# Kernel tuning notes

Hardware: AMD Instinct MI355X
Metric: run time of the kernel (lower is better)

The kernel has to match this reference:

```python
import jax, jax.numpy as jnp
import numpy as np

MEM_SIZE = 2048
CELL = 64
R_HEADS = 4
IN_SIZE = 512
IFACE = CELL * R_HEADS + CELL + 2 * CELL + 2 * R_HEADS + 5  # 461
DELTA = 1e-6
EPS = 1e-6


def setup_inputs() -> dict:
    key = jax.random.key(0)
    ks = jax.random.split(key, 8)
    b = 256
    return {
        'xi': jax.random.normal(ks[0], (b, IN_SIZE), jnp.float32),
        'W': jax.random.normal(ks[1], (IFACE, IN_SIZE), jnp.float32) * 0.05,
        'gamma': jnp.ones((IFACE,), jnp.float32),
        'beta': jnp.zeros((IFACE,), jnp.float32),
        'memory': jax.random.normal(ks[2], (b, MEM_SIZE, CELL), jnp.float32),
        'read_weights': jax.random.uniform(ks[3], (b, R_HEADS, MEM_SIZE), jnp.float32),
        'write_weights': jax.random.uniform(ks[4], (b, 1, MEM_SIZE), jnp.float32),
        'usage': jax.random.uniform(ks[5], (b, MEM_SIZE), jnp.float32),
    }


def _cosine(mem, keys):
    # mem: (b,m,c), keys: (b,k,c) -> (b,k,m)
    mem_n = mem / (jnp.linalg.norm(mem, axis=-1, keepdims=True) + EPS)
    key_n = keys / (jnp.linalg.norm(keys, axis=-1, keepdims=True) + EPS)
    return jnp.einsum('bkc,bmc->bkm', key_n, mem_n)


def reference(xi, W, gamma, beta, memory, read_weights, write_weights, usage):
    b = xi.shape[0]
    r, k, w, m = R_HEADS, CELL, CELL, MEM_SIZE

    # interface projection + GroupNorm(1, C) over channel dim
    itf = xi @ W.T
    mu = jnp.mean(itf, axis=1, keepdims=True)
    var = jnp.var(itf, axis=1, keepdims=True)
    itf = (itf - mu) / jnp.sqrt(var + 1e-5) * gamma + beta

    c = 0
    read_keys = jnp.tanh(itf[:, c:c + r * k].reshape(b, r, k)); c += r * k
    read_strengths = jax.nn.softplus(itf[:, c:c + r]); c += r
    write_key = jnp.tanh(itf[:, c:c + k].reshape(b, 1, k)); c += k
    write_strength = jax.nn.softplus(itf[:, c]).reshape(b, 1); c += 1
    erase_vec = jax.nn.sigmoid(itf[:, c:c + w].reshape(b, 1, w)); c += w
    write_vec = jnp.tanh(itf[:, c:c + w].reshape(b, 1, w)); c += w
    free_gates = jax.nn.sigmoid(itf[:, c:c + r]); c += r
    alloc_gate = jax.nn.softmax(itf[:, c:c + 3], axis=1); c += 3
    write_gate = jax.nn.sigmoid(itf[:, c]).reshape(b, 1)

    # ---- usage update ----
    u = usage + (1 - usage) * (1 - jnp.prod(1 - write_weights, axis=1))
    psi = jnp.prod(1 - free_gates[:, :, None] * read_weights, axis=1)  # (b,m)
    u = u * psi

    # ---- content weighting for write ----
    wcw = jax.nn.softmax(_cosine(memory, write_key) * write_strength[:, :, None], axis=2)  # (b,1,m)

    # ---- allocation ----
    u2 = DELTA + (1 - DELTA) * u
    idx = jnp.argsort(u2, axis=1)                              # ascending usage (phi)
    su = jnp.take_along_axis(u2, idx, axis=1)                  # sorted usage
    cp = jnp.cumprod(jnp.concatenate([jnp.ones((b, 1), u2.dtype), su], axis=1), axis=1)[:, :-1]
    sa = (1 - su) * cp
    inv = jnp.argsort(idx, axis=1)                             # inverse permutation (phi_rev)
    alloc = jnp.take_along_axis(sa, inv, axis=1)               # (b,m)

    # ---- write weighting ----
    fw = (alloc_gate[:, 0:1] * jnp.mean(read_weights, axis=1)
          + alloc_gate[:, 1:2] * alloc
          + alloc_gate[:, 2:3] * wcw[:, 0])
    ww = (write_gate * fw)[:, None, :]                         # (b,1,m)

    # ---- memory write (erase + add) ----
    reset_gate = jnp.prod(1 - ww[:, :, :, None] * erase_vec[:, :, None, :], axis=1)  # (b,m,w)
    mem = memory * reset_gate + jnp.einsum('bm,bw->bmw', ww[:, 0], write_vec[:, 0])

    # ---- read ----
    rw = jax.nn.softmax(_cosine(mem, read_keys) * read_strengths[:, :, None], axis=2)  # (b,r,m)
    read_vectors = jnp.einsum('brm,bmw->brw', rw, mem)         # (b,r,w)
    return read_vectors
```

## Files before the change

### kernel.cpp

```cpp
#include <hip/hip_runtime.h>
#include <math.h>

#define MM    2048
#define CC    64
#define RH    4
#define NIF   461
#define INS   512
#define EPSN  1e-6f

typedef unsigned long long u64;

#define OFF_P     ((size_t)0)
#define OFF_U2    ((size_t)131072)
#define OFF_MRW   ((size_t)655360)
#define OFF_SC    ((size_t)1179648)
#define OFF_ALLOC ((size_t)1703936)
#define OFF_WW    ((size_t)2228224)
#define OFF_PART  ((size_t)2752512)
#define OFF_PSTAT ((size_t)3276800)

__global__ __launch_bounds__(512) void k1_interface(
    const float* __restrict__ xi, const float* __restrict__ W,
    const float* __restrict__ gamma, const float* __restrict__ beta,
    const float* __restrict__ read_w, const float* __restrict__ write_w,
    const float* __restrict__ usage, float* __restrict__ ws)
{
  const int b = blockIdx.x, tid = threadIdx.x;
  const int lane = tid & 63, wid = tid >> 6;
  __shared__ __align__(16) float s_xi[512], s_itf[512], s_act[512];
  __shared__ float sRed[24];

  s_xi[tid] = xi[(size_t)b*INS + tid];
  __syncthreads();

  {
    const float4 x0 = ((const float4*)s_xi)[lane*2];
    const float4 x1 = ((const float4*)s_xi)[lane*2+1];
    for (int col = wid; col < NIF; col += 8) {
      const float4* Wr = (const float4*)(W + (size_t)col*INS);
      float4 a0 = Wr[lane*2], a1 = Wr[lane*2+1];
      float p = a0.x*x0.x + a0.y*x0.y + a0.z*x0.z + a0.w*x0.w
              + a1.x*x1.x + a1.y*x1.y + a1.z*x1.z + a1.w*x1.w;
      #pragma unroll
      for (int off=1; off<64; off<<=1) p += __shfl_xor(p, off);
      if (lane==0) s_itf[col] = p;
    }
  }
  __syncthreads();

  {
    float v = (tid < NIF) ? s_itf[tid] : 0.f;
    float s = v, q = v*v;
    #pragma unroll
    for (int off=1; off<64; off<<=1) { s += __shfl_xor(s,off); q += __shfl_xor(q,off); }
    if (lane==0){ sRed[wid] = s; sRed[8+wid] = q; }
    __syncthreads();
    if (tid==0){
      float ts=0.f, tq=0.f;
      for (int i=0;i<8;i++){ ts+=sRed[i]; tq+=sRed[8+i]; }
      float mean = ts/(float)NIF;
      float var  = tq/(float)NIF - mean*mean;
      sRed[16]=mean; sRed[17]=rsqrtf(var+1e-5f);
    }
    __syncthreads();
    float mean = sRed[16], rstd = sRed[17];
    if (tid < NIF) {
      float g = (s_itf[tid]-mean)*rstd*gamma[tid] + beta[tid];
      float a;
      if      (tid < 256) a = tanhf(g);
      else if (tid < 260) a = fmaxf(g,0.f) + log1pf(expf(-fabsf(g)));
      else if (tid < 324) a = tanhf(g);
      else if (tid ==324) a = fmaxf(g,0.f) + log1pf(expf(-fabsf(g)));
      else if (tid < 389) a = 1.f/(1.f+expf(-g));
      else if (tid < 453) a = tanhf(g);
      else if (tid < 457) a = 1.f/(1.f+expf(-g));
      else if (tid < 460) a = g;
      else                a = 1.f/(1.f+expf(-g));
      s_act[tid] = a;
    }
  }
  __syncthreads();

  float* P = ws + OFF_P + (size_t)b*512;
  if (wid < 4) {
    float t = s_act[wid*64 + lane];
    float q = t*t;
    #pragma unroll
    for (int off=1; off<64; off<<=1) q += __shfl_xor(q,off);
    P[wid*64+lane] = t * (s_act[256+wid] / (sqrtf(q) + EPSN));
  } else if (wid == 4) {
    float t = s_act[260+lane];
    float q = t*t;
    #pragma unroll
    for (int off=1; off<64; off<<=1) q += __shfl_xor(q,off);
    P[256+lane] = t * (s_act[324] / (sqrtf(q) + EPSN));
  } else if (wid == 5) {
    P[320+lane] = s_act[325+lane];
    P[384+lane] = s_act[389+lane];
  } else if (wid == 6 && lane == 0) {
    float a0=s_act[457], a1=s_act[458], a2=s_act[459];
    float mx = fmaxf(a0, fmaxf(a1,a2));
    float e0=expf(a0-mx), e1=expf(a1-mx), e2=expf(a2-mx);
    float is = 1.f/(e0+e1+e2);
    P[448]=e0*is; P[449]=e1*is; P[450]=e2*is; P[451]=s_act[460];
  }

  {
    const float4* us4 = (const float4*)(usage   + (size_t)b*MM);
    const float4* wr4 = (const float4*)(write_w + (size_t)b*MM);
    const float4* rw4 = (const float4*)(read_w  + (size_t)b*RH*MM);
    const float fg0=s_act[453], fg1=s_act[454], fg2=s_act[455], fg3=s_act[456];
    float4 u = us4[tid], w = wr4[tid];
    float4 r0 = rw4[tid], r1 = rw4[512+tid], r2 = rw4[1024+tid], r3 = rw4[1536+tid];
    float4 mr, u2o;
    mr.x = 0.25f*(r0.x+r1.x+r2.x+r3.x);
    mr.y = 0.25f*(r0.y+r1.y+r2.y+r3.y);
    mr.z = 0.25f*(r0.z+r1.z+r2.z+r3.z);
    mr.w = 0.25f*(r0.w+r1.w+r2.w+r3.w);
    #define U2C(comp)                                                           \
    { float uu  = u.comp + (1.f-u.comp)*w.comp;                                 \
      float psi = (1.f-fg0*r0.comp)*(1.f-fg1*r1.comp)*(1.f-fg2*r2.comp)*(1.f-fg3*r3.comp); \
      u2o.comp = 1e-6f + (1.f-1e-6f)*(uu*psi); }
    U2C(x) U2C(y) U2C(z) U2C(w)
    #undef U2C
    ((float4*)(ws + OFF_MRW + (size_t)b*MM))[tid] = mr;
    ((float4*)(ws + OFF_U2  + (size_t)b*MM))[tid] = u2o;
  }
}

__global__ __launch_bounds__(256) void k2_fused(
    const float* __restrict__ memory, float* __restrict__ ws)
{
  __shared__ __align__(16) u64 sKeys[2048];
  __shared__ float sT[260];
  const int tid = threadIdx.x;

  if (blockIdx.x < 256) {
    const int b = blockIdx.x;
    const int lane = tid & 63, w = tid >> 6;
    const float* u2p = ws + OFF_U2 + (size_t)b*MM;
    for (int i = tid; i < MM; i += 256)
      sKeys[i] = ((u64)__float_as_uint(u2p[i])<<32) | (unsigned)i;
    __syncthreads();

    for (int k = 2; k <= MM; k <<= 1) {
      for (int j = k >> 1; j > 0; j >>= 1) {
        #pragma unroll 4
        for (int c = tid; c < MM/2; c += 256) {
          int i   = ((c & ~(j-1)) << 1) | (c & (j-1));
          int ixj = i | j;
          u64 a = sKeys[i], d = sKeys[ixj];
          bool up = ((i & k) == 0);
          if ((a > d) == up) { sKeys[i] = d; sKeys[ixj] = a; }
        }
        __syncthreads();
      }
    }

    float p[8];
    {
      float run = 1.f;
      #pragma unroll
      for (int e = 0; e < 8; ++e) {
        float su = __uint_as_float((unsigned)(sKeys[tid*8+e]>>32));
        run *= su; p[e] = run;
      }
      sT[tid] = run;
    }
    __syncthreads();
    float v = sT[tid];
    float incl = v;
    #pragma unroll
    for (int off=1; off<64; off<<=1) {
      float n = __shfl_up(incl, off);
      if (lane >= off) incl *= n;
    }
    float excl = __shfl_up(incl, 1);
    if (lane == 0) excl = 1.f;
    if (lane == 63) sT[256 + w] = incl;
    __syncthreads();
    float base = 1.f;
    for (int ww2 = 0; ww2 < w; ++ww2) base *= sT[256 + ww2];
    float E = base * excl;

    float* allocp = ws + OFF_ALLOC + (size_t)b*MM;
    #pragma unroll
    for (int e = 0; e < 8; ++e) {
      u64 kk = sKeys[tid*8+e];
      float su = __uint_as_float((unsigned)(kk>>32));
      unsigned idx = (unsigned)(kk & 0xFFFFFFFFu);
      float cp = E * (e ? p[e-1] : 1.f);
      allocp[idx] = (1.f - su) * cp;
    }
  } else {
    const int f = blockIdx.x - 256;
    const int b = f >> 3, slice = f & 7;
    const int l16 = tid & 15, rowg = tid >> 4;
    const float* P = ws + OFF_P + (size_t)b*512;
    const float4 wk4 = ((const float4*)(P+256))[l16];
    const float4* mem4 = (const float4*)(memory + (size_t)b*MM*CC) + (size_t)slice*256*16;
    float* sc = ws + OFF_SC + (size_t)b*MM + slice*256;
    #pragma unroll 4
    for (int it = 0; it < 16; ++it) {
      int m = it*16 + rowg;
      float4 vv = mem4[m*16 + l16];
      float d = vv.x*wk4.x + vv.y*wk4.y + vv.z*wk4.z + vv.w*wk4.w;
      float q = vv.x*vv.x + vv.y*vv.y + vv.z*vv.z + vv.w*vv.w;
      #pragma unroll
      for (int off=1; off<16; off<<=1){ d += __shfl_xor(d,off); q += __shfl_xor(q,off); }
      if (l16==0) sc[m] = d / (sqrtf(q)+EPSN);
    }
  }
}

__global__ __launch_bounds__(256) void k3_ww(float* __restrict__ ws)
{
  const int b = blockIdx.x, tid = threadIdx.x;
  const int lane = tid & 63, w = tid >> 6;
  __shared__ float sR[8];
  const float4* sc4 = (const float4*)(ws + OFF_SC + (size_t)b*MM);
  float4 v0 = sc4[tid*2], v1 = sc4[tid*2+1];
  float m = fmaxf(fmaxf(fmaxf(v0.x,v0.y),fmaxf(v0.z,v0.w)),
                  fmaxf(fmaxf(v1.x,v1.y),fmaxf(v1.z,v1.w)));
  #pragma unroll
  for (int off=1; off<64; off<<=1) m = fmaxf(m, __shfl_xor(m,off));
  if (lane==0) sR[w] = m;
  __syncthreads();
  m = fmaxf(fmaxf(sR[0],sR[1]), fmaxf(sR[2],sR[3]));
  float e0=expf(v0.x-m), e1=expf(v0.y-m), e2=expf(v0.z-m), e3=expf(v0.w-m);
  float e4=expf(v1.x-m), e5=expf(v1.y-m), e6=expf(v1.z-m), e7=expf(v1.w-m);
  float s = e0+e1+e2+e3+e4+e5+e6+e7;
  #pragma unroll
  for (int off=1; off<64; off<<=1) s += __shfl_xor(s,off);
  if (lane==0) sR[4+w] = s;
  __syncthreads();
  float inv = 1.f/(sR[4]+sR[5]+sR[6]+sR[7]);

  const float* P = ws + OFF_P + (size_t)b*512;
  const float ag0=P[448], ag1=P[449], ag2=P[450], wg=P[451];
  const float4* mr4 = (const float4*)(ws + OFF_MRW   + (size_t)b*MM);
  const float4* al4 = (const float4*)(ws + OFF_ALLOC + (size_t)b*MM);
  float4* ww4 = (float4*)(ws + OFF_WW + (size_t)b*MM);
  float4 mra = mr4[tid*2], mrb = mr4[tid*2+1];
  float4 ala = al4[tid*2], alb = al4[tid*2+1];
  float4 oa, ob;
  oa.x = wg*(ag0*mra.x + ag1*ala.x + ag2*e0*inv);
  oa.y = wg*(ag0*mra.y + ag1*ala.y + ag2*e1*inv);
  oa.z = wg*(ag0*mra.z + ag1*ala.z + ag2*e2*inv);
  oa.w = wg*(ag0*mra.w + ag1*ala.w + ag2*e3*inv);
  ob.x = wg*(ag0*mrb.x + ag1*alb.x + ag2*e4*inv);
  ob.y = wg*(ag0*mrb.y + ag1*alb.y + ag2*e5*inv);
  ob.z = wg*(ag0*mrb.z + ag1*alb.z + ag2*e6*inv);
  ob.w = wg*(ag0*mrb.w + ag1*alb.w + ag2*e7*inv);
  ww4[tid*2] = oa; ww4[tid*2+1] = ob;
}

__global__ __launch_bounds__(256) void k4_passB(
    const float* __restrict__ memory, float* __restrict__ ws)
{
  const int slice = blockIdx.x, b = blockIdx.y;
  const int tid = threadIdx.x, l16 = tid & 15, rowg = tid >> 4;
  const int lane = tid & 63, wid = tid >> 6;
  __shared__ __align__(16) float chunk[64*68];
  __shared__ __align__(16) float sE[4*68];
  __shared__ float sHm[4], sHs[4], sHsc[4];

  const float* P = ws + OFF_P + (size_t)b*512;
  const float4 er4 = ((const float4*)(P+320))[l16];
  const float4 wv4 = ((const float4*)(P+384))[l16];
  const float4 k0 = ((const float4*)P)[     l16];
  const float4 k1 = ((const float4*)P)[16 + l16];
  const float4 k2 = ((const float4*)P)[32 + l16];
  const float4 k3 = ((const float4*)P)[48 + l16];
  const float* wwp = ws + OFF_WW + (size_t)b*MM + slice*256;
  const float4* mem4 = (const float4*)(memory + (size_t)b*MM*CC) + (size_t)slice*256*16;

  if (tid < 4){ sHm[tid] = -INFINITY; sHs[tid] = 0.f; }
  __syncthreads();
  const int q = lane & 15, ps = lane >> 4;
  float4 acc; acc.x=acc.y=acc.z=acc.w=0.f;

  for (int ch = 0; ch < 4; ++ch) {
    #pragma unroll
    for (int pp = 0; pp < 4; ++pp) {
      int p = pp*16 + rowg;
      int m = ch*64 + p;
      float4 v = mem4[m*16 + l16];
      float wm = wwp[m];
      float4 nv;
      nv.x = v.x*(1.f - wm*er4.x) + wm*wv4.x;
      nv.y = v.y*(1.f - wm*er4.y) + wm*wv4.y;
      nv.z = v.z*(1.f - wm*er4.z) + wm*wv4.z;
      nv.w = v.w*(1.f - wm*er4.w) + wm*wv4.w;
      *(float4*)&chunk[p*68 + (l16<<2)] = nv;
      float d0 = nv.x*k0.x+nv.y*k0.y+nv.z*k0.z+nv.w*k0.w;
      float d1 = nv.x*k1.x+nv.y*k1.y+nv.z*k1.z+nv.w*k1.w;
      float d2 = nv.x*k2.x+nv.y*k2.y+nv.z*k2.z+nv.w*k2.w;
      float d3 = nv.x*k3.x+nv.y*k3.y+nv.z*k3.z+nv.w*k3.w;
      float qq = nv.x*nv.x+nv.y*nv.y+nv.z*nv.z+nv.w*nv.w;
      #pragma unroll
      for (int off=1; off<16; off<<=1){
        d0+=__shfl_xor(d0,off); d1+=__shfl_xor(d1,off);
        d2+=__shfl_xor(d2,off); d3+=__shfl_xor(d3,off);
        qq+=__shfl_xor(qq,off);
      }
      if (l16==0){
        float inv = 1.f/(sqrtf(qq)+EPSN);
        sE[      p] = d0*inv;
        sE[ 68 + p] = d1*inv;
        sE[136 + p] = d2*inv;
        sE[204 + p] = d3*inv;
      }
    }
    __syncthreads();
    {
      float v = sE[wid*68 + lane];
      float cm = v;
      #pragma unroll
      for (int off=1; off<64; off<<=1) cm = fmaxf(cm, __shfl_xor(cm,off));
      float om = sHm[wid];
      float nm = fmaxf(om, cm);
      float scl = expf(om - nm);
      float e = expf(v - nm);
      sE[wid*68 + lane] = e;
      float es = e;
      #pragma unroll
      for (int off=1; off<64; off<<=1) es += __shfl_xor(es,off);
      if (lane==0){
        sHs[wid] = sHs[wid]*scl + es;
        sHm[wid] = nm;
        sHsc[wid] = scl;
      }
    }
    __syncthreads();
    {
      float scl = sHsc[wid];
      acc.x*=scl; acc.y*=scl; acc.z*=scl; acc.w*=scl;
      #pragma unroll
      for (int pp = 0; pp < 16; ++pp) {
        int p = ps*16 + pp;
        float e = sE[wid*68 + p];
        const float4 mv = *(const float4*)&chunk[p*68 + (q<<2)];
        acc.x += e*mv.x; acc.y += e*mv.y; acc.z += e*mv.z; acc.w += e*mv.w;
      }
    }
    __syncthreads();
  }

  #pragma unroll
  for (int off=16; off<64; off<<=1) {
    acc.x += __shfl_xor(acc.x, off);
    acc.y += __shfl_xor(acc.y, off);
    acc.z += __shfl_xor(acc.z, off);
    acc.w += __shfl_xor(acc.w, off);
  }
  if (ps == 0) {
    float* pacc = ws + OFF_PART + ((((size_t)b*8 + slice)*4 + wid)<<6);
    *(float4*)&pacc[q<<2] = acc;
  }
  if (lane == 0) {
    float* pst = ws + OFF_PSTAT + (((size_t)b*8 + slice)*4 + wid)*2;
    pst[0] = sHm[wid]; pst[1] = sHs[wid];
  }
}

__global__ __launch_bounds__(256) void k5_combine(
    const float* __restrict__ ws, float* __restrict__ out)
{
  const int b = blockIdx.x, tid = threadIdx.x;
  const int head = tid >> 6, c = tid & 63;
  float M = -INFINITY;
  #pragma unroll
  for (int s = 0; s < 8; ++s)
    M = fmaxf(M, ws[OFF_PSTAT + (((size_t)b*8 + s)*4 + head)*2]);
  float S = 0.f, A = 0.f;
  #pragma unroll
  for (int s = 0; s < 8; ++s) {
    const float* pst = ws + OFF_PSTAT + (((size_t)b*8 + s)*4 + head)*2;
    float w = expf(pst[0] - M);
    S += w * pst[1];
    A += w * ws[OFF_PART + ((((size_t)b*8 + s)*4 + head)<<6) + c];
  }
  out[((size_t)b<<8) + head*64 + c] = A / S;
}

extern "C" void kernel_launch(void* const* d_in, const int* in_sizes, int n_in,
                              void* d_out, int out_size, void* d_ws, size_t ws_size,
                              hipStream_t stream) {
  const float* xi      = (const float*)d_in[0];
  const float* W       = (const float*)d_in[1];
  const float* gamma   = (const float*)d_in[2];
  const float* beta    = (const float*)d_in[3];
  const float* memory  = (const float*)d_in[4];
  const float* read_w  = (const float*)d_in[5];
  const float* write_w = (const float*)d_in[6];
  const float* usage   = (const float*)d_in[7];
  float* ws  = (float*)d_ws;
  float* out = (float*)d_out;

  k1_interface<<<dim3(256), dim3(512), 0, stream>>>(xi, W, gamma, beta, read_w, write_w, usage, ws);
  k2_fused   <<<dim3(2304), dim3(256), 0, stream>>>(memory, ws);
  k3_ww      <<<dim3(256), dim3(256), 0, stream>>>(ws);
  k4_passB   <<<dim3(8,256), dim3(256), 0, stream>>>(memory, ws);
  k5_combine <<<dim3(256), dim3(256), 0, stream>>>(ws, out);
}
```

Baseline: 132.3 us.

## Precompute per-row dot products to derive post-write cosine scores algebraically

The memory-scan kernel now computes, for each memory row, a set of dot products (row with write key, erase-weighted row, write vector and read keys). These let the written memory's norms and read-key cosines be reconstructed from the write weight without building the new memory. A single per-batch kernel then does the full read softmax exactly instead of an online softmax across slices. The final pass becomes a plain weighted reduction of the original memory, and the erase/add terms are applied algebraically in the combine step. This moves arithmetic out of the second memory pass at the cost of a larger per-row scalar buffer and more dot products in the first pass.

```diff
diff --git a/kernel.cpp b/kernel.cpp
--- a/kernel.cpp
+++ b/kernel.cpp
@@ -13,11 +13,11 @@
 #define OFF_P     ((size_t)0)
 #define OFF_U2    ((size_t)131072)
 #define OFF_MRW   ((size_t)655360)
-#define OFF_SC    ((size_t)1179648)
-#define OFF_ALLOC ((size_t)1703936)
-#define OFF_WW    ((size_t)2228224)
-#define OFF_PART  ((size_t)2752512)
-#define OFF_PSTAT ((size_t)3276800)
+#define OFF_ALLOC ((size_t)1179648)
+#define OFF_SCAL  ((size_t)1703936)
+#define OFF_W8    ((size_t)10092544)
+#define OFF_CR    ((size_t)14286848)
+#define OFF_PART  ((size_t)14287872)
 
 __global__ __launch_bounds__(512) void k1_interface(
     const float* __restrict__ xi, const float* __restrict__ W,
@@ -195,172 +195,252 @@
   } else {
     const int f = blockIdx.x - 256;
     const int b = f >> 3, slice = f & 7;
-    const int l16 = tid & 15, rowg = tid >> 4;
+    const int q = tid & 7, rowg = tid >> 3;
     const float* P = ws + OFF_P + (size_t)b*512;
-    const float4 wk4 = ((const float4*)(P+256))[l16];
+    const float4 wkA = ((const float4*)(P+256))[q*2], wkB = ((const float4*)(P+256))[q*2+1];
+    const float4 eA  = ((const float4*)(P+320))[q*2], eB  = ((const float4*)(P+320))[q*2+1];
+    const float4 wvA = ((const float4*)(P+384))[q*2], wvB = ((const float4*)(P+384))[q*2+1];
+    const float4 k0A = ((const float4*)P)[      q*2], k0B = ((const float4*)P)[      q*2+1];
+    const float4 k1A = ((const float4*)P)[ 16 + q*2], k1B = ((const float4*)P)[ 16 + q*2+1];
+    const float4 k2A = ((const float4*)P)[ 32 + q*2], k2B = ((const float4*)P)[ 32 + q*2+1];
+    const float4 k3A = ((const float4*)P)[ 48 + q*2], k3B = ((const float4*)P)[ 48 + q*2+1];
     const float4* mem4 = (const float4*)(memory + (size_t)b*MM*CC) + (size_t)slice*256*16;
-    float* sc = ws + OFF_SC + (size_t)b*MM + slice*256;
-    #pragma unroll 4
-    for (int it = 0; it < 16; ++it) {
-      int m = it*16 + rowg;
-      float4 vv = mem4[m*16 + l16];
-      float d = vv.x*wk4.x + vv.y*wk4.y + vv.z*wk4.z + vv.w*wk4.w;
-      float q = vv.x*vv.x + vv.y*vv.y + vv.z*vv.z + vv.w*vv.w;
+    float4* sc4 = (float4*)(ws + OFF_SCAL) + ((size_t)b*MM + slice*256)*4;
+
+    for (int it = 0; it < 8; ++it) {
+      int m = it*32 + rowg;
+      float4 vA = mem4[m*16 + q*2], vB = mem4[m*16 + q*2+1];
+      float4 veA, veB;
+      veA.x=vA.x*eA.x; veA.y=vA.y*eA.y; veA.z=vA.z*eA.z; veA.w=vA.w*eA.w;
+      veB.x=vB.x*eB.x; veB.y=vB.y*eB.y; veB.z=vB.z*eB.z; veB.w=vB.w*eB.w;
+      #define DOT(a,b) (a.x*b.x + a.y*b.y + a.z*b.z + a.w*b.w)
+      float S  = DOT(vA,wkA) + DOT(vB,wkB);
+      float A  = DOT(vA,vA)  + DOT(vB,vB);
+      float B  = DOT(veA,vA) + DOT(veB,vB);
+      float C  = DOT(veA,veA)+ DOT(veB,veB);
+      float D  = DOT(vA,wvA) + DOT(vB,wvB);
+      float E  = DOT(veA,wvA)+ DOT(veB,wvB);
+      float G0 = DOT(vA,k0A) + DOT(vB,k0B);
+      float G1 = DOT(vA,k1A) + DOT(vB,k1B);
+      float G2 = DOT(vA,k2A) + DOT(vB,k2B);
+      float G3 = DOT(vA,k3A) + DOT(vB,k3B);
+      float H0 = DOT(veA,k0A)+ DOT(veB,k0B);
+      float H1 = DOT(veA,k1A)+ DOT(veB,k1B);
+      float H2 = DOT(veA,k2A)+ DOT(veB,k2B);
+      float H3 = DOT(veA,k3A)+ DOT(veB,k3B);
+      #undef DOT
       #pragma unroll
-      for (int off=1; off<16; off<<=1){ d += __shfl_xor(d,off); q += __shfl_xor(q,off); }
-      if (l16==0) sc[m] = d / (sqrtf(q)+EPSN);
-    }
-  }
-}
-
-__global__ __launch_bounds__(256) void k3_ww(float* __restrict__ ws)
+      for (int off=1; off<8; off<<=1) {
+        S += __shfl_xor(S,off);   A += __shfl_xor(A,off);
+        B += __shfl_xor(B,off);   C += __shfl_xor(C,off);
+        D += __shfl_xor(D,off);   E += __shfl_xor(E,off);
+        G0 += __shfl_xor(G0,off); G1 += __shfl_xor(G1,off);
+        G2 += __shfl_xor(G2,off); G3 += __shfl_xor(G3,off);
+        H0 += __shfl_xor(H0,off); H1 += __shfl_xor(H1,off);
+        H2 += __shfl_xor(H2,off); H3 += __shfl_xor(H3,off);
+      }
+      if (q == 0) {
+        float4 o0; o0.x=S;  o0.y=A;  o0.z=B;  o0.w=C;
+        float4 o1; o1.x=D;  o1.y=E;  o1.z=0;  o1.w=0;
+        float4 o2; o2.x=G0; o2.y=G1; o2.z=G2; o2.w=G3;
+        float4 o3; o3.x=H0; o3.y=H1; o3.z=H2; o3.w=H3;
+        sc4[m*4+0]=o0; sc4[m*4+1]=o1; sc4[m*4+2]=o2; sc4[m*4+3]=o3;
+      }
+    }
+  }
+}
+
+__global__ __launch_bounds__(256) void k3_weights(float* __restrict__ ws)
 {
   const int b = blockIdx.x, tid = threadIdx.x;
   const int lane = tid & 63, w = tid >> 6;
-  __shared__ float sR[8];
-  const float4* sc4 = (const float4*)(ws + OFF_SC + (size_t)b*MM);
-  float4 v0 = sc4[tid*2], v1 = sc4[tid*2+1];
-  float m = fmaxf(fmaxf(fmaxf(v0.x,v0.y),fmaxf(v0.z,v0.w)),
-                  fmaxf(fmaxf(v1.x,v1.y),fmaxf(v1.z,v1.w)));
-  #pragma unroll
-  for (int off=1; off<64; off<<=1) m = fmaxf(m, __shfl_xor(m,off));
-  if (lane==0) sR[w] = m;
-  __syncthreads();
-  m = fmaxf(fmaxf(sR[0],sR[1]), fmaxf(sR[2],sR[3]));
-  float e0=expf(v0.x-m), e1=expf(v0.y-m), e2=expf(v0.z-m), e3=expf(v0.w-m);
-  float e4=expf(v1.x-m), e5=expf(v1.y-m), e6=expf(v1.z-m), e7=expf(v1.w-m);
-  float s = e0+e1+e2+e3+e4+e5+e6+e7;
-  #pragma unroll
-  for (int off=1; off<64; off<<=1) s += __shfl_xor(s,off);
-  if (lane==0) sR[4+w] = s;
-  __syncthreads();
-  float inv = 1.f/(sR[4]+sR[5]+sR[6]+sR[7]);
+  __shared__ float sWraw[2048];
+  __shared__ float sWw[2048];
+  __shared__ float sSc[4*2048];
+  __shared__ float sR[64];
+  __shared__ float sKF[8];
 
   const float* P = ws + OFF_P + (size_t)b*512;
+  const float* scal = ws + OFF_SCAL + (size_t)b*MM*16;
+  const float4* sc4 = (const float4*)scal;
+
+  if (tid < 64) {
+    float wv = P[384+tid];
+    float p0=wv*P[tid], p1=wv*P[64+tid], p2=wv*P[128+tid], p3=wv*P[192+tid], f=wv*wv;
+    #pragma unroll
+    for (int off=1; off<64; off<<=1) {
+      p0+=__shfl_xor(p0,off); p1+=__shfl_xor(p1,off); p2+=__shfl_xor(p2,off);
+      p3+=__shfl_xor(p3,off); f+=__shfl_xor(f,off);
+    }
+    if (tid==0){ sKF[0]=p0; sKF[1]=p1; sKF[2]=p2; sKF[3]=p3; sKF[4]=f; }
+  }
+  __syncthreads();
+
+  float lm = -INFINITY;
+  #pragma unroll
+  for (int k = 0; k < 8; ++k) {
+    int m = tid + k*256;
+    float4 s0 = sc4[m*4];
+    float wraw = s0.x / (sqrtf(s0.y)+EPSN);
+    sWraw[m] = wraw;
+    lm = fmaxf(lm, wraw);
+  }
+  #pragma unroll
+  for (int off=1; off<64; off<<=1) lm = fmaxf(lm, __shfl_xor(lm,off));
+  if (lane==0) sR[w] = lm;
+  __syncthreads();
+  const float Mw = fmaxf(fmaxf(sR[0],sR[1]), fmaxf(sR[2],sR[3]));
+  float ls = 0.f;
+  #pragma unroll
+  for (int k = 0; k < 8; ++k) ls += expf(sWraw[tid + k*256] - Mw);
+  #pragma unroll
+  for (int off=1; off<64; off<<=1) ls += __shfl_xor(ls,off);
+  if (lane==0) sR[4+w] = ls;
+  __syncthreads();
+  const float invW = 1.f/(sR[4]+sR[5]+sR[6]+sR[7]);
+
   const float ag0=P[448], ag1=P[449], ag2=P[450], wg=P[451];
-  const float4* mr4 = (const float4*)(ws + OFF_MRW   + (size_t)b*MM);
-  const float4* al4 = (const float4*)(ws + OFF_ALLOC + (size_t)b*MM);
-  float4* ww4 = (float4*)(ws + OFF_WW + (size_t)b*MM);
-  float4 mra = mr4[tid*2], mrb = mr4[tid*2+1];
-  float4 ala = al4[tid*2], alb = al4[tid*2+1];
-  float4 oa, ob;
-  oa.x = wg*(ag0*mra.x + ag1*ala.x + ag2*e0*inv);
-  oa.y = wg*(ag0*mra.y + ag1*ala.y + ag2*e1*inv);
-  oa.z = wg*(ag0*mra.z + ag1*ala.z + ag2*e2*inv);
-  oa.w = wg*(ag0*mra.w + ag1*ala.w + ag2*e3*inv);
-  ob.x = wg*(ag0*mrb.x + ag1*alb.x + ag2*e4*inv);
-  ob.y = wg*(ag0*mrb.y + ag1*alb.y + ag2*e5*inv);
-  ob.z = wg*(ag0*mrb.z + ag1*alb.z + ag2*e6*inv);
-  ob.w = wg*(ag0*mrb.w + ag1*alb.w + ag2*e7*inv);
-  ww4[tid*2] = oa; ww4[tid*2+1] = ob;
-}
-
-__global__ __launch_bounds__(256) void k4_passB(
-    const float* __restrict__ memory, float* __restrict__ ws)
+  const float K0=sKF[0], K1=sKF[1], K2=sKF[2], K3=sKF[3], F=sKF[4];
+  const float* mrwp = ws + OFF_MRW   + (size_t)b*MM;
+  const float* alp  = ws + OFF_ALLOC + (size_t)b*MM;
+
+  float hm0=-INFINITY, hm1=-INFINITY, hm2=-INFINITY, hm3=-INFINITY;
+  #pragma unroll
+  for (int k = 0; k < 8; ++k) {
+    int m = tid + k*256;
+    float wcw = expf(sWraw[m]-Mw)*invW;
+    float wwv = wg*(ag0*mrwp[m] + ag1*alp[m] + ag2*wcw);
+    sWw[m] = wwv;
+    float4 s0 = sc4[m*4], s1 = sc4[m*4+1], sG = sc4[m*4+2], sH = sc4[m*4+3];
+    float nsq = s0.y + 2.f*wwv*(s1.x - s0.z) + wwv*wwv*(s0.w - 2.f*s1.y + F);
+    float rstd = 1.f/(sqrtf(fmaxf(nsq,0.f))+EPSN);
+    float c0 = (sG.x + wwv*(K0 - sH.x))*rstd;
+    float c1 = (sG.y + wwv*(K1 - sH.y))*rstd;
+    float c2 = (sG.z + wwv*(K2 - sH.z))*rstd;
+    float c3 = (sG.w + wwv*(K3 - sH.w))*rstd;
+    sSc[       m] = c0; sSc[2048 + m] = c1;
+    sSc[4096 + m] = c2; sSc[6144 + m] = c3;
+    hm0=fmaxf(hm0,c0); hm1=fmaxf(hm1,c1); hm2=fmaxf(hm2,c2); hm3=fmaxf(hm3,c3);
+  }
+  #pragma unroll
+  for (int off=1; off<64; off<<=1) {
+    hm0=fmaxf(hm0,__shfl_xor(hm0,off)); hm1=fmaxf(hm1,__shfl_xor(hm1,off));
+    hm2=fmaxf(hm2,__shfl_xor(hm2,off)); hm3=fmaxf(hm3,__shfl_xor(hm3,off));
+  }
+  if (lane==0){ sR[8+w*4]=hm0; sR[9+w*4]=hm1; sR[10+w*4]=hm2; sR[11+w*4]=hm3; }
+  __syncthreads();
+  const float M0 = fmaxf(fmaxf(sR[8], sR[12]), fmaxf(sR[16], sR[20]));
+  const float M1 = fmaxf(fmaxf(sR[9], sR[13]), fmaxf(sR[17], sR[21]));
+  const float M2 = fmaxf(fmaxf(sR[10],sR[14]), fmaxf(sR[18], sR[22]));
+  const float M3 = fmaxf(fmaxf(sR[11],sR[15]), fmaxf(sR[19], sR[23]));
+  float h0=0.f,h1=0.f,h2=0.f,h3=0.f;
+  #pragma unroll
+  for (int k = 0; k < 8; ++k) {
+    int m = tid + k*256;
+    h0 += expf(sSc[       m]-M0); h1 += expf(sSc[2048 + m]-M1);
+    h2 += expf(sSc[4096 + m]-M2); h3 += expf(sSc[6144 + m]-M3);
+  }
+  #pragma unroll
+  for (int off=1; off<64; off<<=1) {
+    h0+=__shfl_xor(h0,off); h1+=__shfl_xor(h1,off);
+    h2+=__shfl_xor(h2,off); h3+=__shfl_xor(h3,off);
+  }
+  if (lane==0){ sR[24+w*4]=h0; sR[25+w*4]=h1; sR[26+w*4]=h2; sR[27+w*4]=h3; }
+  __syncthreads();
+  const float i0 = 1.f/(sR[24]+sR[28]+sR[32]+sR[36]);
+  const float i1 = 1.f/(sR[25]+sR[29]+sR[33]+sR[37]);
+  const float i2 = 1.f/(sR[26]+sR[30]+sR[34]+sR[38]);
+  const float i3 = 1.f/(sR[27]+sR[31]+sR[35]+sR[39]);
+  float4* w84 = (float4*)(ws + OFF_W8 + (size_t)b*MM*8);
+  float cr0=0.f, cr1=0.f, cr2=0.f, cr3=0.f;
+  #pragma unroll
+  for (int k = 0; k < 8; ++k) {
+    int m = tid + k*256;
+    float wwv = sWw[m];
+    float a0 = expf(sSc[       m]-M0)*i0;
+    float a1 = expf(sSc[2048 + m]-M1)*i1;
+    float a2 = expf(sSc[4096 + m]-M2)*i2;
+    float a3 = expf(sSc[6144 + m]-M3)*i3;
+    float4 oa; oa.x=a0; oa.y=a1; oa.z=a2; oa.w=a3;
+    float4 og; og.x=a0*wwv; og.y=a1*wwv; og.z=a2*wwv; og.w=a3*wwv;
+    w84[m*2] = oa; w84[m*2+1] = og;
+    cr0 += og.x; cr1 += og.y; cr2 += og.z; cr3 += og.w;
+  }
+  #pragma unroll
+  for (int off=1; off<64; off<<=1) {
+    cr0+=__shfl_xor(cr0,off); cr1+=__shfl_xor(cr1,off);
+    cr2+=__shfl_xor(cr2,off); cr3+=__shfl_xor(cr3,off);
+  }
+  if (lane==0){ sR[40+w*4]=cr0; sR[41+w*4]=cr1; sR[42+w*4]=cr2; sR[43+w*4]=cr3; }
+  __syncthreads();
+  if (tid < 4)
+    ws[OFF_CR + (size_t)b*4 + tid] =
+      sR[40+tid] + sR[44+tid] + sR[48+tid] + sR[52+tid];
+}
+
+__global__ __launch_bounds__(256) void k4_reduce(
+    const float* __restrict__ memory, const float* __restrict__ ws,
+    float* __restrict__ wso)
 {
   const int slice = blockIdx.x, b = blockIdx.y;
-  const int tid = threadIdx.x, l16 = tid & 15, rowg = tid >> 4;
-  const int lane = tid & 63, wid = tid >> 6;
-  __shared__ __align__(16) float chunk[64*68];
-  __shared__ __align__(16) float sE[4*68];
-  __shared__ float sHm[4], sHs[4], sHsc[4];
-
-  const float* P = ws + OFF_P + (size_t)b*512;
-  const float4 er4 = ((const float4*)(P+320))[l16];
-  const float4 wv4 = ((const float4*)(P+384))[l16];
-  const float4 k0 = ((const float4*)P)[     l16];
-  const float4 k1 = ((const float4*)P)[16 + l16];
-  const float4 k2 = ((const float4*)P)[32 + l16];
-  const float4 k3 = ((const float4*)P)[48 + l16];
-  const float* wwp = ws + OFF_WW + (size_t)b*MM + slice*256;
+  const int tid = threadIdx.x;
+  const int w = tid >> 6, lane = tid & 63;
+  const int rq = lane >> 4, cq = lane & 15;
+  __shared__ __align__(16) float ldsW8[256*8];
+  __shared__ __align__(16) float ldsP[4*16*32];
+
+  {
+    const float4* g = (const float4*)(ws + OFF_W8 + ((size_t)b*MM + slice*256)*8);
+    ((float4*)ldsW8)[tid] = g[tid];
+    ((float4*)ldsW8)[tid+256] = g[tid+256];
+  }
+  __syncthreads();
+
   const float4* mem4 = (const float4*)(memory + (size_t)b*MM*CC) + (size_t)slice*256*16;
-
-  if (tid < 4){ sHm[tid] = -INFINITY; sHs[tid] = 0.f; }
-  __syncthreads();
-  const int q = lane & 15, ps = lane >> 4;
-  float4 acc; acc.x=acc.y=acc.z=acc.w=0.f;
-
-  for (int ch = 0; ch < 4; ++ch) {
-    #pragma unroll
-    for (int pp = 0; pp < 4; ++pp) {
-      int p = pp*16 + rowg;
-      int m = ch*64 + p;
-      float4 v = mem4[m*16 + l16];
-      float wm = wwp[m];
-      float4 nv;
-      nv.x = v.x*(1.f - wm*er4.x) + wm*wv4.x;
-      nv.y = v.y*(1.f - wm*er4.y) + wm*wv4.y;
-      nv.z = v.z*(1.f - wm*er4.z) + wm*wv4.z;
-      nv.w = v.w*(1.f - wm*er4.w) + wm*wv4.w;
-      *(float4*)&chunk[p*68 + (l16<<2)] = nv;
-      float d0 = nv.x*k0.x+nv.y*k0.y+nv.z*k0.z+nv.w*k0.w;
-      float d1 = nv.x*k1.x+nv.y*k1.y+nv.z*k1.z+nv.w*k1.w;
-      float d2 = nv.x*k2.x+nv.y*k2.y+nv.z*k2.z+nv.w*k2.w;
-      float d3 = nv.x*k3.x+nv.y*k3.y+nv.z*k3.z+nv.w*k3.w;
-      float qq = nv.x*nv.x+nv.y*nv.y+nv.z*nv.z+nv.w*nv.w;
-      #pragma unroll
-      for (int off=1; off<16; off<<=1){
-        d0+=__shfl_xor(d0,off); d1+=__shfl_xor(d1,off);
-        d2+=__shfl_xor(d2,off); d3+=__shfl_xor(d3,off);
-        qq+=__shfl_xor(qq,off);
-      }
-      if (l16==0){
-        float inv = 1.f/(sqrtf(qq)+EPSN);
-        sE[      p] = d0*inv;
-        sE[ 68 + p] = d1*inv;
-        sE[136 + p] = d2*inv;
-        sE[204 + p] = d3*inv;
-      }
-    }
-    __syncthreads();
-    {
-      float v = sE[wid*68 + lane];
-      float cm = v;
-      #pragma unroll
-      for (int off=1; off<64; off<<=1) cm = fmaxf(cm, __shfl_xor(cm,off));
-      float om = sHm[wid];
-      float nm = fmaxf(om, cm);
-      float scl = expf(om - nm);
-      float e = expf(v - nm);
-      sE[wid*68 + lane] = e;
-      float es = e;
-      #pragma unroll
-      for (int off=1; off<64; off<<=1) es += __shfl_xor(es,off);
-      if (lane==0){
-        sHs[wid] = sHs[wid]*scl + es;
-        sHm[wid] = nm;
-        sHsc[wid] = scl;
-      }
-    }
-    __syncthreads();
-    {
-      float scl = sHsc[wid];
-      acc.x*=scl; acc.y*=scl; acc.z*=scl; acc.w*=scl;
-      #pragma unroll
-      for (int pp = 0; pp < 16; ++pp) {
-        int p = ps*16 + pp;
-        float e = sE[wid*68 + p];
-        const float4 mv = *(const float4*)&chunk[p*68 + (q<<2)];
-        acc.x += e*mv.x; acc.y += e*mv.y; acc.z += e*mv.z; acc.w += e*mv.w;
-      }
-    }
-    __syncthreads();
-  }
-
-  #pragma unroll
-  for (int off=16; off<64; off<<=1) {
-    acc.x += __shfl_xor(acc.x, off);
-    acc.y += __shfl_xor(acc.y, off);
-    acc.z += __shfl_xor(acc.z, off);
-    acc.w += __shfl_xor(acc.w, off);
-  }
-  if (ps == 0) {
-    float* pacc = ws + OFF_PART + ((((size_t)b*8 + slice)*4 + wid)<<6);
-    *(float4*)&pacc[q<<2] = acc;
-  }
-  if (lane == 0) {
-    float* pst = ws + OFF_PSTAT + (((size_t)b*8 + slice)*4 + wid)*2;
-    pst[0] = sHm[wid]; pst[1] = sHs[wid];
+  float4 acc[8];
+  #pragma unroll
+  for (int j=0;j<8;++j){ acc[j].x=0;acc[j].y=0;acc[j].z=0;acc[j].w=0; }
+
+  #pragma unroll 4
+  for (int i = 0; i < 16; ++i) {
+    int m = w*64 + i*4 + rq;
+    float4 v = mem4[m*16 + cq];
+    float4 wa = *(const float4*)&ldsW8[m*8];
+    float4 wb = *(const float4*)&ldsW8[m*8+4];
+    #define ACC(j, s) { acc[j].x += (s)*v.x; acc[j].y += (s)*v.y; acc[j].z += (s)*v.z; acc[j].w += (s)*v.w; }
+    ACC(0, wa.x) ACC(1, wa.y) ACC(2, wa.z) ACC(3, wa.w)
+    ACC(4, wb.x) ACC(5, wb.y) ACC(6, wb.z) ACC(7, wb.w)
+    #undef ACC
+  }
+  #pragma unroll
+  for (int j=0;j<8;++j){
+    #pragma unroll
+    for (int off=16; off<64; off<<=1) {
+      acc[j].x += __shfl_xor(acc[j].x, off);
+      acc[j].y += __shfl_xor(acc[j].y, off);
+      acc[j].z += __shfl_xor(acc[j].z, off);
+      acc[j].w += __shfl_xor(acc[j].w, off);
+    }
+  }
+  if (rq == 0) {
+    float4* p4 = (float4*)&ldsP[(w*16 + cq)*32];
+    #pragma unroll
+    for (int j=0;j<8;++j) p4[j] = acc[j];
+  }
+  __syncthreads();
+  {
+    int jj = tid >> 6;
+    int c  = tid & 63;
+    int cq2 = c >> 2, ci = c & 3;
+    float s1 = 0.f, s2 = 0.f;
+    #pragma unroll
+    for (int g=0; g<4; ++g) {
+      s1 += ldsP[(g*16 + cq2)*32 +  jj*4    + ci];
+      s2 += ldsP[(g*16 + cq2)*32 + (jj+4)*4 + ci];
+    }
+    float* part = wso + OFF_PART + (((size_t)b*8 + slice)*8)*64;
+    part[ jj   *64 + c] = s1;
+    part[(jj+4)*64 + c] = s2;
   }
 }
 
@@ -368,20 +448,19 @@
     const float* __restrict__ ws, float* __restrict__ out)
 {
   const int b = blockIdx.x, tid = threadIdx.x;
-  const int head = tid >> 6, c = tid & 63;
-  float M = -INFINITY;
-  #pragma unroll
-  for (int s = 0; s < 8; ++s)
-    M = fmaxf(M, ws[OFF_PSTAT + (((size_t)b*8 + s)*4 + head)*2]);
-  float S = 0.f, A = 0.f;
+  const int h = tid >> 6, c = tid & 63;
+  const float* P = ws + OFF_P + (size_t)b*512;
+  float S1 = 0.f, S2 = 0.f;
   #pragma unroll
   for (int s = 0; s < 8; ++s) {
-    const float* pst = ws + OFF_PSTAT + (((size_t)b*8 + s)*4 + head)*2;
-    float w = expf(pst[0] - M);
-    S += w * pst[1];
-    A += w * ws[OFF_PART + ((((size_t)b*8 + s)*4 + head)<<6) + c];
-  }
-  out[((size_t)b<<8) + head*64 + c] = A / S;
+    const float* part = ws + OFF_PART + (((size_t)b*8 + s)*8)*64;
+    S1 += part[ h   *64 + c];
+    S2 += part[(h+4)*64 + c];
+  }
+  float e  = P[320+c];
+  float wv = P[384+c];
+  float cr = ws[OFF_CR + (size_t)b*4 + h];
+  out[((size_t)b<<8) + h*64 + c] = S1 - e*S2 + cr*wv;
 }
 
 extern "C" void kernel_launch(void* const* d_in, const int* in_sizes, int n_in,
@@ -400,7 +479,7 @@
 
   k1_interface<<<dim3(256), dim3(512), 0, stream>>>(xi, W, gamma, beta, read_w, write_w, usage, ws);
   k2_fused   <<<dim3(2304), dim3(256), 0, stream>>>(memory, ws);
-  k3_ww      <<<dim3(256), dim3(256), 0, stream>>>(ws);
-  k4_passB   <<<dim3(8,256), dim3(256), 0, stream>>>(memory, ws);
+  k3_weights <<<dim3(256), dim3(256), 0, stream>>>(ws);
+  k4_reduce  <<<dim3(8,256), dim3(256), 0, stream>>>(memory, ws, ws);
   k5_combine <<<dim3(256), dim3(256), 0, stream>>>(ws, out);
 }
```

Measured after the change: 138.8 us. 1.05x slower.
